# Optimization experiments

Measured on AMD Instinct MI355X. Metric: run time of the kernel, lower is better.

## Reference

```python
import jax, jax.numpy as jnp
import numpy as np

H = 2048   # hidden_size
K = 2048   # key_size
Q = 2048   # query_size
S = 8192   # source sequence length
V = 2048   # value feature dim


def setup_inputs() -> dict:
    key = jax.random.key(0)
    ks = jax.random.split(key, 6)
    query = jax.random.normal(ks[0], (1, 1, Q), dtype=jnp.float32)
    src_key = jax.random.normal(ks[1], (1, S, K), dtype=jnp.float32)
    values = jax.random.normal(ks[2], (S, V), dtype=jnp.float32)
    # nn.Linear weights are [out, in]; all bias-free
    Wq = jax.random.normal(ks[3], (H, Q), dtype=jnp.float32) / np.sqrt(Q)
    Wk = jax.random.normal(ks[4], (H, K), dtype=jnp.float32) / np.sqrt(K)
    Ws = jax.random.normal(ks[5], (1, H), dtype=jnp.float32) / np.sqrt(H)
    return {"query": query, "key": src_key, "values": values,
            "Wq": Wq, "Wk": Wk, "Ws": Ws}


def reference(query, key, values, Wq, Wk, Ws):
    # projected_query: [1,1,H]; projected_key: [1,S,H]
    pq = jnp.einsum('btq,hq->bth', query, Wq)
    pk = jnp.einsum('bsk,hk->bsh', key, Wk)
    # additive (Bahdanau) scores: [1,S,1] -> squeeze(2).unsqueeze(1) -> [1,1,S]
    scores = jnp.einsum('bsh,oh->bso', jnp.tanh(pq + pk), Ws)
    scores = scores[:, :, 0][:, None, :]
    attention_weights = jax.nn.softmax(scores, axis=-1)        # [1,1,S]
    # bmm([1,1,S], values.unsqueeze(0)=[1,S,V]) -> [1,1,V]
    context = jnp.einsum('bts,sv->btv', attention_weights, values)
    return (attention_weights, context)
```

## Files before the change

### kernel.cpp

```cpp
#include <hip/hip_runtime.h>
#include <hip/hip_bf16.h>
#include <math.h>

#define HDIM 2048
#define KDIM 2048
#define SDIM 8192
#define VDIM 2048
#define BKT  64
#define NT   (KDIM / BKT)

using short8 = __attribute__((ext_vector_type(8))) short;
using f32x4  = __attribute__((ext_vector_type(4))) float;
using us8    = __attribute__((ext_vector_type(8))) unsigned short;

typedef const __attribute__((address_space(1))) void g_void;
typedef __attribute__((address_space(3))) void lds_void;

__device__ __forceinline__ unsigned short f2bf(float f) {
  union { float f; unsigned int u; } x; x.f = f;
  unsigned int r = x.u + 0x7fffu + ((x.u >> 16) & 1u);
  return (unsigned short)(r >> 16);
}

__device__ __forceinline__ float tanh_fast(float x) {
  float e = __expf(2.0f * x);
  return 1.0f - 2.0f * __builtin_amdgcn_rcpf(e + 1.0f);
}

__device__ __forceinline__ void barrier_sync() {
  asm volatile("" ::: "memory");
  __builtin_amdgcn_s_barrier();
  asm volatile("" ::: "memory");
}

__global__ __launch_bounds__(256) void cvt_pq_kernel(const float* __restrict__ key,
                                                     const float* __restrict__ Wk,
                                                     unsigned short* __restrict__ outbf,
                                                     const float* __restrict__ query,
                                                     const float* __restrict__ Wq,
                                                     float* __restrict__ pq,
                                                     int keyN8, int cvtBlocks) {
  if ((int)blockIdx.x < cvtBlocks) {
    int i = blockIdx.x * 256 + threadIdx.x;
    const float* src = (i < keyN8) ? &key[(size_t)i * 8] : &Wk[((size_t)i - keyN8) * 8];
    f32x4 a = *(const f32x4*)src;
    f32x4 b = *(const f32x4*)(src + 4);
    us8 o;
    #pragma unroll
    for (int j = 0; j < 4; ++j) { o[j] = f2bf(a[j]); o[j + 4] = f2bf(b[j]); }
    *(us8*)&outbf[(size_t)i * 8] = o;
  } else {
    int wave = threadIdx.x >> 6, lane = threadIdx.x & 63;
    int h = (blockIdx.x - cvtBlocks) * 4 + wave;
    const float* w = Wq + (size_t)h * KDIM;
    f32x4 s4 = (f32x4)(0.0f);
    #pragma unroll
    for (int i = 0; i < KDIM / 256; ++i) {
      f32x4 q4 = *(const f32x4*)&query[lane * 4 + i * 256];
      f32x4 w4 = *(const f32x4*)&w[lane * 4 + i * 256];
      #pragma unroll
      for (int j = 0; j < 4; ++j) s4[j] = fmaf(q4[j], w4[j], s4[j]);
    }
    float s = s4[0] + s4[1] + s4[2] + s4[3];
    #pragma unroll
    for (int off = 32; off; off >>= 1) s += __shfl_xor(s, off);
    if (lane == 0) pq[h] = s;
  }
}

__global__ __launch_bounds__(512, 2) void scores_kernel(const unsigned short* __restrict__ keybf,
                                                        const unsigned short* __restrict__ wkbf,
                                                        const float* __restrict__ pq,
                                                        const float* __restrict__ Ws,
                                                        float* __restrict__ partial) {
  __shared__ unsigned short lds[65536];

  const int tid = threadIdx.x;
  const int bid = blockIdx.x;
  const int xg = bid & 7, xi = bid >> 3;
  const int bx = xg * 4 + (xi & 3);
  const int by = xi >> 2;
  const int s0 = bx * 256, h0 = by * 256;

  const int wave = tid >> 6, lane = tid & 63;
  const int wm = wave >> 2, wn = wave & 3;
  const int l16 = lane & 15, g16 = lane >> 4;

  const int srow = tid >> 3;
  const int scol = ((tid & 7) * 16) ^ ((srow & 7) << 4);
  const char* aSrc0 = (const char*)keybf + ((size_t)(s0 + srow) * KDIM) * 2 + scol;
  const char* bSrc0 = (const char*)wkbf  + ((size_t)(h0 + srow) * KDIM) * 2 + scol;

  #define STAGE_A(o, kt, buf) __builtin_amdgcn_global_load_lds( \
      (g_void*)(aSrc0 + (size_t)(o) * 64 * KDIM * 2 + (size_t)(kt) * 128), \
      (lds_void*)((char*)lds + (size_t)(buf) * 65536 + (o) * 8192 + wave * 1024), 16, 0, 0)
  #define STAGE_B(o, kt, buf) __builtin_amdgcn_global_load_lds( \
      (g_void*)(bSrc0 + (size_t)(o) * 64 * KDIM * 2 + (size_t)(kt) * 128), \
      (lds_void*)((char*)lds + (size_t)(buf) * 65536 + 32768 + (o) * 8192 + wave * 1024), 16, 0, 0)

  const int xorv = (l16 & 7) << 4;
  int colx[2];
  colx[0] = ((g16 * 16)      ) ^ xorv;
  colx[1] = ((g16 * 16) | 64 ) ^ xorv;
  const int aRowBase = (wm * 128 + l16) * 128;
  const int bRowBase = 32768 + (wn * 64 + l16) * 128;

  f32x4 acc[8][4];
  #pragma unroll
  for (int m = 0; m < 8; ++m)
    #pragma unroll
    for (int n = 0; n < 4; ++n) acc[m][n] = (f32x4)(0.0f);

  STAGE_A(0, 0, 0); STAGE_A(1, 0, 0); STAGE_A(2, 0, 0); STAGE_A(3, 0, 0);
  STAGE_B(0, 0, 0); STAGE_B(1, 0, 0); STAGE_B(2, 0, 0); STAGE_B(3, 0, 0);
  asm volatile("s_waitcnt vmcnt(0)" ::: "memory");
  barrier_sync();

  short8 af[4][2], bf_[4][2];

  for (int t = 0; t < NT; ++t) {
    const int cbase = (t & 1) * 65536;
    const int nbuf = (t & 1) ^ 1;
    const bool more = (t + 1 < NT);

    #pragma unroll
    for (int m = 0; m < 4; ++m)
      #pragma unroll
      for (int ks = 0; ks < 2; ++ks)
        af[m][ks] = *(const short8*)((const char*)lds + cbase + aRowBase + m * 2048 + colx[ks]);
    #pragma unroll
    for (int n = 0; n < 4; ++n)
      #pragma unroll
      for (int ks = 0; ks < 2; ++ks)
        bf_[n][ks] = *(const short8*)((const char*)lds + cbase + bRowBase + n * 2048 + colx[ks]);

    if (more) {
      STAGE_A(0, t + 1, nbuf); STAGE_A(1, t + 1, nbuf);
      STAGE_A(2, t + 1, nbuf); STAGE_A(3, t + 1, nbuf);
      STAGE_B(0, t + 1, nbuf); STAGE_B(1, t + 1, nbuf);
      STAGE_B(2, t + 1, nbuf); STAGE_B(3, t + 1, nbuf);
    }

    __builtin_amdgcn_s_setprio(1);
    #pragma unroll
    for (int ks = 0; ks < 2; ++ks)
      #pragma unroll
      for (int m = 0; m < 4; ++m)
        #pragma unroll
        for (int n = 0; n < 4; ++n)
          acc[m][n] = __builtin_amdgcn_mfma_f32_16x16x32_bf16(af[m][ks], bf_[n][ks], acc[m][n], 0, 0, 0);
    __builtin_amdgcn_s_setprio(0);

    #pragma unroll
    for (int m = 0; m < 4; ++m)
      #pragma unroll
      for (int ks = 0; ks < 2; ++ks)
        af[m][ks] = *(const short8*)((const char*)lds + cbase + aRowBase + (m + 4) * 2048 + colx[ks]);

    __builtin_amdgcn_s_setprio(1);
    #pragma unroll
    for (int ks = 0; ks < 2; ++ks)
      #pragma unroll
      for (int m = 0; m < 4; ++m)
        #pragma unroll
        for (int n = 0; n < 4; ++n)
          acc[m + 4][n] = __builtin_amdgcn_mfma_f32_16x16x32_bf16(af[m][ks], bf_[n][ks], acc[m + 4][n], 0, 0, 0);
    __builtin_amdgcn_s_setprio(0);

    asm volatile("s_waitcnt vmcnt(0)" ::: "memory");
    barrier_sync();
  }

  float pqv[4], wsv[4];
  #pragma unroll
  for (int n = 0; n < 4; ++n) {
    int h = h0 + wn * 64 + n * 16 + l16;
    pqv[n] = pq[h];
    wsv[n] = Ws[h];
  }

  float* sred = (float*)lds;
  #pragma unroll
  for (int m = 0; m < 8; ++m) {
    #pragma unroll
    for (int j = 0; j < 4; ++j) {
      float rs = 0.f;
      #pragma unroll
      for (int n = 0; n < 4; ++n)
        rs += tanh_fast(acc[m][n][j] + pqv[n]) * wsv[n];
      rs += __shfl_xor(rs, 1);
      rs += __shfl_xor(rs, 2);
      rs += __shfl_xor(rs, 4);
      rs += __shfl_xor(rs, 8);
      if (l16 == 0)
        sred[(wm * 128 + m * 16 + g16 * 4 + j) * 4 + wn] = rs;
    }
  }
  __syncthreads();
  if (tid < 256) {
    float v = sred[tid * 4 + 0] + sred[tid * 4 + 1] + sred[tid * 4 + 2] + sred[tid * 4 + 3];
    partial[(size_t)(s0 + tid) * 8 + by] = v;
  }
}

__global__ __launch_bounds__(1024) void softmax_kernel(const float* __restrict__ partial,
                                                       float* __restrict__ weights) {
  __shared__ float red[16];
  int tid = threadIdx.x;
  int sbase = tid * 8;
  float sc[8];
  float mx = -1e30f;
  #pragma unroll
  for (int i = 0; i < 8; ++i) {
    const float* p = partial + (size_t)(sbase + i) * 8;
    float v = 0.f;
    #pragma unroll
    for (int q = 0; q < 8; ++q) v += p[q];
    sc[i] = v;
    mx = fmaxf(mx, v);
  }
  #pragma unroll
  for (int off = 32; off; off >>= 1) mx = fmaxf(mx, __shfl_xor(mx, off));
  if ((tid & 63) == 0) red[tid >> 6] = mx;
  __syncthreads();
  float gmx = red[0];
  #pragma unroll
  for (int q = 1; q < 16; ++q) gmx = fmaxf(gmx, red[q]);
  __syncthreads();
  float ls = 0.f;
  #pragma unroll
  for (int i = 0; i < 8; ++i) { sc[i] = expf(sc[i] - gmx); ls += sc[i]; }
  #pragma unroll
  for (int off = 32; off; off >>= 1) ls += __shfl_xor(ls, off);
  if ((tid & 63) == 0) red[tid >> 6] = ls;
  __syncthreads();
  float gs = 0.f;
  #pragma unroll
  for (int q = 0; q < 16; ++q) gs += red[q];
  float inv = 1.0f / gs;
  #pragma unroll
  for (int i = 0; i < 8; ++i) weights[sbase + i] = sc[i] * inv;
}

__global__ __launch_bounds__(256) void ctx_partial_kernel(const float* __restrict__ values,
                                                          const float* __restrict__ w,
                                                          float* __restrict__ part) {
  int vcol4 = blockIdx.x * 256 + threadIdx.x;
  int ss0 = blockIdx.y * 64;
  f32x4 acc = (f32x4)(0.0f);
  for (int s = ss0; s < ss0 + 64; ++s) {
    f32x4 v = *(const f32x4*)&values[(size_t)s * VDIM + vcol4 * 4];
    float ws = w[s];
    #pragma unroll
    for (int j = 0; j < 4; ++j) acc[j] = fmaf(ws, v[j], acc[j]);
  }
  *(f32x4*)&part[(size_t)blockIdx.y * VDIM + vcol4 * 4] = acc;
}

__global__ __launch_bounds__(256) void ctx_reduce_kernel(const float* __restrict__ part,
                                                         float* __restrict__ ctx) {
  int vcol = blockIdx.x * 256 + threadIdx.x;
  float acc = 0.f;
  #pragma unroll
  for (int p = 0; p < 128; ++p) acc += part[(size_t)p * VDIM + vcol];
  ctx[vcol] = acc;
}

extern "C" void kernel_launch(void* const* d_in, const int* in_sizes, int n_in,
                              void* d_out, int out_size, void* d_ws, size_t ws_size,
                              hipStream_t stream) {
  const float* query  = (const float*)d_in[0];
  const float* key    = (const float*)d_in[1];
  const float* values = (const float*)d_in[2];
  const float* Wq     = (const float*)d_in[3];
  const float* Wk     = (const float*)d_in[4];
  const float* Ws     = (const float*)d_in[5];

  float* out     = (float*)d_out;
  float* weights = out;
  float* ctx     = out + SDIM;

  char* ws = (char*)d_ws;
  unsigned short* keybf = (unsigned short*)ws;
  unsigned short* wkbf  = (unsigned short*)(ws + (size_t)SDIM * KDIM * 2);
  char* tail = ws + (size_t)SDIM * KDIM * 2 + (size_t)HDIM * KDIM * 2;
  float* pq      = (float*)tail;
  float* partial = (float*)(tail + 8192);
  float* cpart   = (float*)(tail + 8192 + (size_t)SDIM * 8 * 4);

  const int keyN8 = SDIM * KDIM / 8;
  const int totN8 = keyN8 + HDIM * KDIM / 8;
  const int cvtBlocks = totN8 / 256;
  cvt_pq_kernel<<<cvtBlocks + HDIM / 4, 256, 0, stream>>>(key, Wk, keybf, query, Wq, pq,
                                                          keyN8, cvtBlocks);
  scores_kernel<<<256, 512, 0, stream>>>(keybf, wkbf, pq, Ws, partial);
  softmax_kernel<<<1, 1024, 0, stream>>>(partial, weights);
  ctx_partial_kernel<<<dim3(VDIM / (256 * 4), 128), 256, 0, stream>>>(values, weights, cpart);
  ctx_reduce_kernel<<<VDIM / 256, 256, 0, stream>>>(cpart, ctx);
}
```

Baseline: 136.1 us.

## Switch scores GEMM to triple-buffered LDS ring with K-tile of 32

Halves the K-tile depth to 32 and replaces the double buffer with a three-slot LDS ring, so global-to-LDS prefetch runs two tiles ahead. A and B stages are issued in separate halves of the iteration with partial vmcnt waits, aiming to hide global latency better and cut LDS use from 128KB to 96KB. In exchange there are twice as many iterations and four barriers per iteration instead of one, which may add sync overhead.

Result: slower. 142.9 us (+5.0%).

```diff
diff --git a/kernel.cpp b/kernel.cpp
--- a/kernel.cpp
+++ b/kernel.cpp
@@ -6,8 +6,10 @@
 #define KDIM 2048
 #define SDIM 8192
 #define VDIM 2048
-#define BKT  64
+#define BKT  32
 #define NT   (KDIM / BKT)
+#define BUFSZ 32768
+#define RING  98304
 
 using short8 = __attribute__((ext_vector_type(8))) short;
 using f32x4  = __attribute__((ext_vector_type(4))) float;
@@ -73,7 +75,7 @@
                                                         const float* __restrict__ pq,
                                                         const float* __restrict__ Ws,
                                                         float* __restrict__ partial) {
-  __shared__ unsigned short lds[65536];
+  __shared__ unsigned short lds[RING / 2];
 
   const int tid = threadIdx.x;
   const int bid = blockIdx.x;
@@ -86,24 +88,21 @@
   const int wm = wave >> 2, wn = wave & 3;
   const int l16 = lane & 15, g16 = lane >> 4;
 
-  const int srow = tid >> 3;
-  const int scol = ((tid & 7) * 16) ^ ((srow & 7) << 4);
-  const char* aSrc0 = (const char*)keybf + ((size_t)(s0 + srow) * KDIM) * 2 + scol;
-  const char* bSrc0 = (const char*)wkbf  + ((size_t)(h0 + srow) * KDIM) * 2 + scol;
-
-  #define STAGE_A(o, kt, buf) __builtin_amdgcn_global_load_lds( \
-      (g_void*)(aSrc0 + (size_t)(o) * 64 * KDIM * 2 + (size_t)(kt) * 128), \
-      (lds_void*)((char*)lds + (size_t)(buf) * 65536 + (o) * 8192 + wave * 1024), 16, 0, 0)
-  #define STAGE_B(o, kt, buf) __builtin_amdgcn_global_load_lds( \
-      (g_void*)(bSrc0 + (size_t)(o) * 64 * KDIM * 2 + (size_t)(kt) * 128), \
-      (lds_void*)((char*)lds + (size_t)(buf) * 65536 + 32768 + (o) * 8192 + wave * 1024), 16, 0, 0)
-
-  const int xorv = (l16 & 7) << 4;
-  int colx[2];
-  colx[0] = ((g16 * 16)      ) ^ xorv;
-  colx[1] = ((g16 * 16) | 64 ) ^ xorv;
-  const int aRowBase = (wm * 128 + l16) * 128;
-  const int bRowBase = 32768 + (wn * 64 + l16) * 128;
+  const int srow = tid >> 2;
+  const int schunk = (tid & 3) ^ ((tid >> 3) & 3);
+  const char* aSrc0 = (const char*)keybf + ((size_t)(s0 + srow) * KDIM) * 2 + schunk * 16;
+  const char* bSrc0 = (const char*)wkbf  + ((size_t)(h0 + srow) * KDIM) * 2 + schunk * 16;
+
+  #define STAGE_A(o, kt, nb) __builtin_amdgcn_global_load_lds( \
+      (g_void*)(aSrc0 + (size_t)(o) * 128 * KDIM * 2 + (size_t)(kt) * 64), \
+      (lds_void*)((char*)lds + (nb) + (o) * 8192 + wave * 1024), 16, 0, 0)
+  #define STAGE_B(o, kt, nb) __builtin_amdgcn_global_load_lds( \
+      (g_void*)(bSrc0 + (size_t)(o) * 128 * KDIM * 2 + (size_t)(kt) * 64), \
+      (lds_void*)((char*)lds + (nb) + 16384 + (o) * 8192 + wave * 1024), 16, 0, 0)
+
+  const int colx = (g16 * 16) ^ (((l16 >> 1) & 3) << 4);
+  const int aRowBase = (wm * 128 + l16) * 64;
+  const int bRowBase = 16384 + (wn * 64 + l16) * 64;
 
   f32x4 acc[8][4];
   #pragma unroll
@@ -111,64 +110,55 @@
     #pragma unroll
     for (int n = 0; n < 4; ++n) acc[m][n] = (f32x4)(0.0f);
 
-  STAGE_A(0, 0, 0); STAGE_A(1, 0, 0); STAGE_A(2, 0, 0); STAGE_A(3, 0, 0);
-  STAGE_B(0, 0, 0); STAGE_B(1, 0, 0); STAGE_B(2, 0, 0); STAGE_B(3, 0, 0);
-  asm volatile("s_waitcnt vmcnt(0)" ::: "memory");
+  STAGE_A(0, 0, 0); STAGE_A(1, 0, 0); STAGE_B(0, 0, 0); STAGE_B(1, 0, 0);
+  STAGE_A(0, 1, BUFSZ); STAGE_A(1, 1, BUFSZ); STAGE_B(0, 1, BUFSZ); STAGE_B(1, 1, BUFSZ);
+  asm volatile("s_waitcnt vmcnt(4)" ::: "memory");
   barrier_sync();
 
-  short8 af[4][2], bf_[4][2];
+  int cb = 0;
+
+  short8 a_[4], b_[4];
 
   for (int t = 0; t < NT; ++t) {
-    const int cbase = (t & 1) * 65536;
-    const int nbuf = (t & 1) ^ 1;
-    const bool more = (t + 1 < NT);
-
-    #pragma unroll
-    for (int m = 0; m < 4; ++m)
-      #pragma unroll
-      for (int ks = 0; ks < 2; ++ks)
-        af[m][ks] = *(const short8*)((const char*)lds + cbase + aRowBase + m * 2048 + colx[ks]);
+    int nb = cb + 2 * BUFSZ; if (nb >= RING) nb -= RING;
+    const bool more2 = (t + 2 < NT);
+
+    #pragma unroll
+    for (int m = 0; m < 4; ++m)
+      a_[m] = *(const short8*)((const char*)lds + cb + aRowBase + m * 1024 + colx);
     #pragma unroll
     for (int n = 0; n < 4; ++n)
-      #pragma unroll
-      for (int ks = 0; ks < 2; ++ks)
-        bf_[n][ks] = *(const short8*)((const char*)lds + cbase + bRowBase + n * 2048 + colx[ks]);
-
-    if (more) {
-      STAGE_A(0, t + 1, nbuf); STAGE_A(1, t + 1, nbuf);
-      STAGE_A(2, t + 1, nbuf); STAGE_A(3, t + 1, nbuf);
-      STAGE_B(0, t + 1, nbuf); STAGE_B(1, t + 1, nbuf);
-      STAGE_B(2, t + 1, nbuf); STAGE_B(3, t + 1, nbuf);
-    }
-
+      b_[n] = *(const short8*)((const char*)lds + cb + bRowBase + n * 1024 + colx);
+    if (more2) { STAGE_A(0, t + 2, nb); STAGE_A(1, t + 2, nb); }
+    barrier_sync();
     __builtin_amdgcn_s_setprio(1);
     #pragma unroll
-    for (int ks = 0; ks < 2; ++ks)
-      #pragma unroll
-      for (int m = 0; m < 4; ++m)
-        #pragma unroll
-        for (int n = 0; n < 4; ++n)
-          acc[m][n] = __builtin_amdgcn_mfma_f32_16x16x32_bf16(af[m][ks], bf_[n][ks], acc[m][n], 0, 0, 0);
+    for (int m = 0; m < 4; ++m)
+      #pragma unroll
+      for (int n = 0; n < 4; ++n)
+        acc[m][n] = __builtin_amdgcn_mfma_f32_16x16x32_bf16(a_[m], b_[n], acc[m][n], 0, 0, 0);
     __builtin_amdgcn_s_setprio(0);
-
-    #pragma unroll
-    for (int m = 0; m < 4; ++m)
-      #pragma unroll
-      for (int ks = 0; ks < 2; ++ks)
-        af[m][ks] = *(const short8*)((const char*)lds + cbase + aRowBase + (m + 4) * 2048 + colx[ks]);
-
+    barrier_sync();
+
+    #pragma unroll
+    for (int m = 0; m < 4; ++m)
+      a_[m] = *(const short8*)((const char*)lds + cb + aRowBase + (m + 4) * 1024 + colx);
+    if (more2) { STAGE_B(0, t + 2, nb); STAGE_B(1, t + 2, nb); }
+    barrier_sync();
     __builtin_amdgcn_s_setprio(1);
     #pragma unroll
-    for (int ks = 0; ks < 2; ++ks)
-      #pragma unroll
-      for (int m = 0; m < 4; ++m)
-        #pragma unroll
-        for (int n = 0; n < 4; ++n)
-          acc[m + 4][n] = __builtin_amdgcn_mfma_f32_16x16x32_bf16(af[m][ks], bf_[n][ks], acc[m + 4][n], 0, 0, 0);
+    for (int m = 0; m < 4; ++m)
+      #pragma unroll
+      for (int n = 0; n < 4; ++n)
+        acc[m + 4][n] = __builtin_amdgcn_mfma_f32_16x16x32_bf16(a_[m], b_[n], acc[m + 4][n], 0, 0, 0);
     __builtin_amdgcn_s_setprio(0);
-
-    asm volatile("s_waitcnt vmcnt(0)" ::: "memory");
-    barrier_sync();
+    if (more2)
+      asm volatile("s_waitcnt vmcnt(4)" ::: "memory");
+    else
+      asm volatile("s_waitcnt vmcnt(0)" ::: "memory");
+    barrier_sync();
+
+    cb += BUFSZ; if (cb >= RING) cb = 0;
   }
 
   float pqv[4], wsv[4];
```

## Split softmax into blockwise partials and fuse normalization into context reduction

Applied to the files above, without the earlier changes.

Replaces the single-block softmax plus two-stage context kernels with a 32-block partial softmax that writes unnormalized exponentials and per-block max/sum pairs. A fused context kernel then combines the pairs, writes the normalized weights, and reduces over all of S within each block, dropping the separate reduce kernel and its partial buffer. It also marks the one-shot fp32 reads in the convert kernel as nontemporal loads. The trade-off is that each context block now walks all 8192 rows for only 8 columns (256 blocks), so the access pattern and parallelism change.

Result: faster. 126.6 us, median of 2 (-7.0%).

```diff
diff --git a/kernel.cpp b/kernel.cpp
--- a/kernel.cpp
+++ b/kernel.cpp
@@ -43,8 +43,8 @@
   if ((int)blockIdx.x < cvtBlocks) {
     int i = blockIdx.x * 256 + threadIdx.x;
     const float* src = (i < keyN8) ? &key[(size_t)i * 8] : &Wk[((size_t)i - keyN8) * 8];
-    f32x4 a = *(const f32x4*)src;
-    f32x4 b = *(const f32x4*)(src + 4);
+    f32x4 a = __builtin_nontemporal_load((const f32x4*)src);
+    f32x4 b = __builtin_nontemporal_load((const f32x4*)(src + 4));
     us8 o;
     #pragma unroll
     for (int j = 0; j < 4; ++j) { o[j] = f2bf(a[j]); o[j + 4] = f2bf(b[j]); }
@@ -57,7 +57,7 @@
     #pragma unroll
     for (int i = 0; i < KDIM / 256; ++i) {
       f32x4 q4 = *(const f32x4*)&query[lane * 4 + i * 256];
-      f32x4 w4 = *(const f32x4*)&w[lane * 4 + i * 256];
+      f32x4 w4 = __builtin_nontemporal_load((const f32x4*)&w[lane * 4 + i * 256]);
       #pragma unroll
       for (int j = 0; j < 4; ++j) s4[j] = fmaf(q4[j], w4[j], s4[j]);
     }
@@ -203,67 +203,84 @@
   }
 }
 
-__global__ __launch_bounds__(1024) void softmax_kernel(const float* __restrict__ partial,
-                                                       float* __restrict__ weights) {
-  __shared__ float red[16];
-  int tid = threadIdx.x;
-  int sbase = tid * 8;
-  float sc[8];
-  float mx = -1e30f;
-  #pragma unroll
-  for (int i = 0; i < 8; ++i) {
-    const float* p = partial + (size_t)(sbase + i) * 8;
-    float v = 0.f;
-    #pragma unroll
-    for (int q = 0; q < 8; ++q) v += p[q];
-    sc[i] = v;
-    mx = fmaxf(mx, v);
-  }
+__global__ __launch_bounds__(256) void smax_part_kernel(const float* __restrict__ partial,
+                                                        float* __restrict__ wexp,
+                                                        float* __restrict__ pairs) {
+  __shared__ float red[8];
+  int tid = threadIdx.x, wave = tid >> 6, lane = tid & 63;
+  int s = blockIdx.x * 256 + tid;
+  const float* p = partial + (size_t)s * 8;
+  float v = 0.f;
+  #pragma unroll
+  for (int q = 0; q < 8; ++q) v += p[q];
+  float mx = v;
   #pragma unroll
   for (int off = 32; off; off >>= 1) mx = fmaxf(mx, __shfl_xor(mx, off));
-  if ((tid & 63) == 0) red[tid >> 6] = mx;
-  __syncthreads();
-  float gmx = red[0];
-  #pragma unroll
-  for (int q = 1; q < 16; ++q) gmx = fmaxf(gmx, red[q]);
-  __syncthreads();
-  float ls = 0.f;
-  #pragma unroll
-  for (int i = 0; i < 8; ++i) { sc[i] = expf(sc[i] - gmx); ls += sc[i]; }
-  #pragma unroll
-  for (int off = 32; off; off >>= 1) ls += __shfl_xor(ls, off);
-  if ((tid & 63) == 0) red[tid >> 6] = ls;
-  __syncthreads();
+  if (lane == 0) red[wave] = mx;
+  __syncthreads();
+  float bmax = fmaxf(fmaxf(red[0], red[1]), fmaxf(red[2], red[3]));
+  float e = __expf(v - bmax);
+  wexp[s] = e;
+  float sm = e;
+  #pragma unroll
+  for (int off = 32; off; off >>= 1) sm += __shfl_xor(sm, off);
+  if (lane == 0) red[4 + wave] = sm;
+  __syncthreads();
+  if (tid == 0)
+    { pairs[blockIdx.x * 2] = bmax; pairs[blockIdx.x * 2 + 1] = red[4] + red[5] + red[6] + red[7]; }
+}
+
+__global__ __launch_bounds__(256) void ctx_fused_kernel(const float* __restrict__ values,
+                                                        const float* __restrict__ wexp,
+                                                        const float* __restrict__ pairs,
+                                                        float* __restrict__ weights,
+                                                        float* __restrict__ ctx) {
+  __shared__ float scl[32];
+  __shared__ f32x4 sred[256];
+  int tid = threadIdx.x, b = blockIdx.x;
+
+  float gmax = -1e30f;
+  #pragma unroll
+  for (int i = 0; i < 32; ++i) gmax = fmaxf(gmax, pairs[2 * i]);
   float gs = 0.f;
   #pragma unroll
-  for (int q = 0; q < 16; ++q) gs += red[q];
+  for (int i = 0; i < 32; ++i) gs += pairs[2 * i + 1] * __expf(pairs[2 * i] - gmax);
+  if (tid < 32) scl[tid] = __expf(pairs[2 * tid] - gmax);
+  __syncthreads();
   float inv = 1.0f / gs;
-  #pragma unroll
-  for (int i = 0; i < 8; ++i) weights[sbase + i] = sc[i] * inv;
-}
-
-__global__ __launch_bounds__(256) void ctx_partial_kernel(const float* __restrict__ values,
-                                                          const float* __restrict__ w,
-                                                          float* __restrict__ part) {
-  int vcol4 = blockIdx.x * 256 + threadIdx.x;
-  int ss0 = blockIdx.y * 64;
+
+  if (b < 32) {
+    int s = b * 256 + tid;
+    weights[s] = wexp[s] * scl[b] * inv;
+  }
+
+  const int c4 = b * 2 + (tid & 1);
+  const int g  = tid >> 1;
   f32x4 acc = (f32x4)(0.0f);
-  for (int s = ss0; s < ss0 + 64; ++s) {
-    f32x4 v = *(const f32x4*)&values[(size_t)s * VDIM + vcol4 * 4];
-    float ws = w[s];
-    #pragma unroll
-    for (int j = 0; j < 4; ++j) acc[j] = fmaf(ws, v[j], acc[j]);
-  }
-  *(f32x4*)&part[(size_t)blockIdx.y * VDIM + vcol4 * 4] = acc;
-}
-
-__global__ __launch_bounds__(256) void ctx_reduce_kernel(const float* __restrict__ part,
-                                                         float* __restrict__ ctx) {
-  int vcol = blockIdx.x * 256 + threadIdx.x;
-  float acc = 0.f;
-  #pragma unroll
-  for (int p = 0; p < 128; ++p) acc += part[(size_t)p * VDIM + vcol];
-  ctx[vcol] = acc;
+  for (int s = g; s < SDIM; s += 128) {
+    float w = wexp[s] * scl[s >> 8];
+    f32x4 v = *(const f32x4*)&values[(size_t)s * VDIM + c4 * 4];
+    #pragma unroll
+    for (int j = 0; j < 4; ++j) acc[j] = fmaf(w, v[j], acc[j]);
+  }
+  sred[tid] = acc;
+  #pragma unroll
+  for (int step = 64; step; step >>= 1) {
+    __syncthreads();
+    if (g < step) {
+      f32x4 a = sred[tid], o = sred[tid + step * 2];
+      #pragma unroll
+      for (int j = 0; j < 4; ++j) a[j] += o[j];
+      sred[tid] = a;
+    }
+  }
+  __syncthreads();
+  if (tid < 2) {
+    f32x4 a = sred[tid];
+    #pragma unroll
+    for (int j = 0; j < 4; ++j) a[j] *= inv;
+    *(f32x4*)&ctx[(size_t)(b * 2 + tid) * 4] = a;
+  }
 }
 
 extern "C" void kernel_launch(void* const* d_in, const int* in_sizes, int n_in,
@@ -286,7 +303,8 @@
   char* tail = ws + (size_t)SDIM * KDIM * 2 + (size_t)HDIM * KDIM * 2;
   float* pq      = (float*)tail;
   float* partial = (float*)(tail + 8192);
-  float* cpart   = (float*)(tail + 8192 + (size_t)SDIM * 8 * 4);
+  float* wexp    = (float*)(tail + 8192 + (size_t)SDIM * 8 * 4);
+  float* pairs   = wexp + SDIM;
 
   const int keyN8 = SDIM * KDIM / 8;
   const int totN8 = keyN8 + HDIM * KDIM / 8;
@@ -294,7 +312,6 @@
   cvt_pq_kernel<<<cvtBlocks + HDIM / 4, 256, 0, stream>>>(key, Wk, keybf, query, Wq, pq,
                                                           keyN8, cvtBlocks);
   scores_kernel<<<256, 512, 0, stream>>>(keybf, wkbf, pq, Ws, partial);
-  softmax_kernel<<<1, 1024, 0, stream>>>(partial, weights);
-  ctx_partial_kernel<<<dim3(VDIM / (256 * 4), 128), 256, 0, stream>>>(values, weights, cpart);
-  ctx_reduce_kernel<<<VDIM / 256, 256, 0, stream>>>(cpart, ctx);
-}
+  smax_part_kernel<<<32, 256, 0, stream>>>(partial, wexp, pairs);
+  ctx_fused_kernel<<<256, 256, 0, stream>>>(values, wexp, pairs, weights, ctx);
+}
```
